# Kernel tuning notes

Measured on AMD Instinct MI355X. Metric: run time of the kernel, lower is better.

The kernel has to match this reference:

```python
import jax, jax.numpy as jnp
import numpy as np

TEMP = 0.5
EPS = 1e-12  # torch F.normalize eps


def setup_inputs() -> dict:
    key = jax.random.key(0)
    k1, k2, k3 = jax.random.split(key, 3)
    B, D = 2048, 128
    z = jax.random.normal(k1, (B, D), dtype=jnp.float32)
    z_aug = jax.random.normal(k2, (B, D), dtype=jnp.float32)
    labels = jax.random.randint(k3, (B,), 0, 2, dtype=jnp.int64)
    return {"z": z, "z_aug": z_aug, "labels": labels}


def _l2_normalize(x):
    n = jnp.linalg.norm(x, axis=1, keepdims=True)
    return x / jnp.maximum(n, EPS)


def _pucon_loss(z, z_aug, labels):
    B = z.shape[0]
    z = _l2_normalize(z)
    z_aug = _l2_normalize(z_aug)

    s00 = (z @ z.T) / TEMP          # [B, B]
    s01 = (z @ z_aug.T) / TEMP
    s10 = (z_aug @ z.T) / TEMP
    s11 = (z_aug @ z_aug.T) / TEMP

    eye = jnp.eye(B, dtype=bool)

    # ---- SelfSupConLoss (reduction='none'): CE over rows with own-diagonal
    # removed from the 00/11 blocks; removal == masking with -inf for CE.
    neg_inf = jnp.array(-jnp.inf, dtype=s00.dtype)
    logits = jnp.concatenate([
        jnp.concatenate([s01, jnp.where(eye, neg_inf, s00)], axis=1),
        jnp.concatenate([s10, jnp.where(eye, neg_inf, s11)], axis=1),
    ], axis=0)                       # [2B, 2B]
    pos = jnp.concatenate([jnp.diagonal(s01), jnp.diagonal(s10)])  # [2B]
    lse = jax.scipy.special.logsumexp(logits, axis=1)
    unsup = lse - pos                # [2B] per-sample NT-Xent loss

    # ---- SupConLoss (reduction='none')
    M = jnp.concatenate([
        jnp.concatenate([s00, s01], axis=1),
        jnp.concatenate([s10, s11], axis=1),
    ], axis=0)                       # [2B, 2B]
    mx = jax.lax.stop_gradient(jnp.max(M, axis=1, keepdims=True))
    Ms = M - mx
    mask = ~jnp.eye(2 * B, dtype=bool)
    e = jnp.where(mask, jnp.exp(Ms), 0.0)
    denom = jnp.sum(e, axis=1, keepdims=True)
    # -log(exp(Ms)/denom) on off-diagonal entries, 0 on diagonal
    nll = jnp.where(mask, jnp.log(denom) - Ms, 0.0)
    eq = labels[:, None] == labels[None, :]
    eq2 = jnp.tile(eq, (2, 2))       # [2B, 2B] bool
    sup = jnp.sum(nll * eq2, axis=1) / (jnp.sum(eq2, axis=1) - 1)  # [2B]

    # ---- PU combination: positives use sup loss, unlabeled use unsup loss
    lab2 = jnp.tile(labels, 2)       # [2B]
    pos_m = (lab2 == 1)
    neg_m = (lab2 == 0)
    n_p = jnp.sum(pos_m)
    n_u = jnp.sum(neg_m)
    total = jnp.maximum(n_p + n_u, 1)
    loss = (jnp.sum(jnp.where(pos_m, sup, 0.0)) +
            jnp.sum(jnp.where(neg_m, unsup, 0.0))) / total
    return jnp.where(n_p == 0, jnp.mean(unsup), loss)


def reference(z, z_aug, labels):
    return _pucon_loss(z, z_aug, labels)
```

## Files before the change

### kernel.cpp

```cpp
#include <hip/hip_runtime.h>
#include <hip/hip_bf16.h>

#define Bsz 2048
#define Dim 128
#define Nrows 4096

typedef float f32x4 __attribute__((ext_vector_type(4)));
typedef __bf16 bf16x8 __attribute__((ext_vector_type(8)));


__global__ __launch_bounds__(256) void k_norm(const float* __restrict__ z,
                                              const float* __restrict__ za,
                                              const long long* __restrict__ labels,
                                              __bf16* __restrict__ U,
                                              float* __restrict__ w1p,
                                              float* __restrict__ wallp,
                                              int* __restrict__ c1out) {
    const int wid = threadIdx.x >> 6, lane = threadIdx.x & 63;
    __shared__ float s1[4][128];
    __shared__ float s0[4][128];
    float a1x = 0.f, a1y = 0.f, a0x = 0.f, a0y = 0.f;
    #pragma unroll
    for (int pass = 0; pass < 4; pass++) {
        const int r = blockIdx.x * 16 + pass * 4 + wid;
        const float* src = (r < Bsz) ? (z + (size_t)r * Dim) : (za + (size_t)(r - Bsz) * Dim);
        float2 x = reinterpret_cast<const float2*>(src)[lane];
        float ss = x.x * x.x + x.y * x.y;
        #pragma unroll
        for (int m = 1; m < 64; m <<= 1) ss += __shfl_xor(ss, m);
        const float sc = 1.0f / fmaxf(sqrtf(ss), 1e-12f);
        const float u0 = x.x * sc, u1 = x.y * sc;
        __bf16* dst = U + (size_t)r * Dim + 2 * lane;
        dst[0] = (__bf16)u0;
        dst[1] = (__bf16)u1;
        const float lf = (labels[r & (Bsz - 1)] == 1) ? 1.f : 0.f;
        a0x += u0; a0y += u1;
        a1x = fmaf(lf, u0, a1x); a1y = fmaf(lf, u1, a1y);
    }
    s1[wid][2 * lane] = a1x; s1[wid][2 * lane + 1] = a1y;
    s0[wid][2 * lane] = a0x; s0[wid][2 * lane + 1] = a0y;
    __syncthreads();
    const int t = threadIdx.x;
    if (t < 128) {
        w1p[blockIdx.x * 128 + t]   = s1[0][t] + s1[1][t] + s1[2][t] + s1[3][t];
        wallp[blockIdx.x * 128 + t] = s0[0][t] + s0[1][t] + s0[2][t] + s0[3][t];
    }
    if (blockIdx.x == 0) {
        __shared__ int ci[256];
        int c = 0;
        #pragma unroll
        for (int k = 0; k < 8; k++) c += (int)labels[t * 8 + k];
        ci[t] = c;
        __syncthreads();
        for (int s = 128; s > 0; s >>= 1) {
            if (t < s) ci[t] += ci[t + s];
            __syncthreads();
        }
        if (t == 0) c1out[0] = ci[0];
    }
}

__global__ __launch_bounds__(512, 2) void k_gram(const __bf16* __restrict__ U,
                                                 const float* __restrict__ w1p,
                                                 const float* __restrict__ wallp,
                                                 float* __restrict__ part,
                                                 float* __restrict__ w1,
                                                 float* __restrict__ wall) {
    if (blockIdx.x == 0) {
        const int t = threadIdx.x;
        if (t < 256) {
            const int d = t & 127;
            const float* src = (t < 128) ? w1p : wallp;
            float acc = 0.f;
            #pragma unroll 8
            for (int k = 0; k < 256; k++) acc += src[k * 128 + d];
            if (t < 128) w1[d] = acc; else wall[d] = acc;
        }
        return;
    }

    __shared__ __bf16 Ai[256 * 128];
    __shared__ __bf16 Aj[256 * 128];

    const int ibk = (blockIdx.x - 1) >> 4, jbk = (blockIdx.x - 1) & 15;
    const bool diag = (ibk == jbk);
    const int ibase = ibk * 256, jbase = jbk * 256;
    const int w = threadIdx.x >> 6, lane = threadIdx.x & 63;
    const int wiq = w & 3, wjh = w >> 2;
    const int l15 = lane & 15, l4 = lane >> 4;

    {
        const int p = lane & 15, rsub = lane >> 4;
        bf16x8 sti[8], stj[8];
        #pragma unroll
        for (int it = 0; it < 8; it++) {
            const int rl = w * 32 + it * 4 + rsub;
            sti[it] = *reinterpret_cast<const bf16x8*>(U + (size_t)(ibase + rl) * Dim + p * 8);
        }
        if (!diag) {
            #pragma unroll
            for (int it = 0; it < 8; it++) {
                const int rl = w * 32 + it * 4 + rsub;
                stj[it] = *reinterpret_cast<const bf16x8*>(U + (size_t)(jbase + rl) * Dim + p * 8);
            }
        }
        #pragma unroll
        for (int it = 0; it < 8; it++) {
            const int rl = w * 32 + it * 4 + rsub;
            *reinterpret_cast<bf16x8*>(Ai + (rl * 16 + (p ^ (rl & 7))) * 8) = sti[it];
        }
        if (!diag) {
            #pragma unroll
            for (int it = 0; it < 8; it++) {
                const int rl = w * 32 + it * 4 + rsub;
                *reinterpret_cast<bf16x8*>(Aj + (rl * 16 + (p ^ (rl & 7))) * 8) = stj[it];
            }
        }
    }
    __syncthreads();
    const __bf16* AjP = diag ? Ai : Aj;

    bf16x8 b[4][4];
    #pragma unroll
    for (int bt = 0; bt < 4; bt++)
        #pragma unroll
        for (int ks = 0; ks < 4; ks++) {
            const int row = wiq * 64 + bt * 16 + l15;
            b[bt][ks] = *reinterpret_cast<const bf16x8*>(
                Ai + (row * 16 + ((ks * 4 + l4) ^ (row & 7))) * 8);
        }

    float dsum[4] = {0.f, 0.f, 0.f, 0.f};
    const float KE1 = 2.8853900817779268f;
    const float KE0 = -2.8853900817779268f;

    #pragma unroll
    for (int at = 0; at < 8; at++) {
        const int arow = wjh * 128 + at * 16 + l15;
        bf16x8 a[4];
        #pragma unroll
        for (int ks = 0; ks < 4; ks++)
            a[ks] = *reinterpret_cast<const bf16x8*>(
                AjP + (arow * 16 + ((ks * 4 + l4) ^ (arow & 7))) * 8);
        const int jt = jbase + wjh * 128 + at * 16;

        #pragma unroll
        for (int bt = 0; bt < 4; bt++) {
            f32x4 acc = {0.f, 0.f, 0.f, 0.f};
            #pragma unroll
            for (int ks = 0; ks < 4; ks++)
                acc = __builtin_amdgcn_mfma_f32_16x16x32_bf16(a[ks], b[bt][ks], acc, 0, 0, 0);
            const bool dg = (jt == ibase + wiq * 64 + bt * 16);
            #pragma unroll
            for (int q = 0; q < 4; q++) {
                float e = exp2f(fmaf(acc[q], KE1, KE0));
                if (dg && (l15 == l4 * 4 + q)) e = 0.f;
                dsum[bt] += e;
            }
        }
    }

    const int strip = jbk * 2 + wjh;
    #pragma unroll
    for (int bt = 0; bt < 4; bt++) {
        float v0 = dsum[bt];
        v0 += __shfl_xor(v0, 16);
        v0 += __shfl_xor(v0, 32);
        if (l4 == 0)
            part[(ibase + wiq * 64 + bt * 16 + l15) * 32 + strip] = v0;
    }
}

__global__ __launch_bounds__(256) void k_row(const __bf16* __restrict__ U,
                                             const long long* __restrict__ labels,
                                             const int* __restrict__ c1p,
                                             const float* __restrict__ part,
                                             const float* __restrict__ w1,
                                             const float* __restrict__ wall,
                                             float* __restrict__ rowC,
                                             float* __restrict__ rowU) {
    const int wid = threadIdx.x >> 6, lane = threadIdx.x & 63;
    const int ls = lane & 31;
    const int c1 = *c1p;
    const float w1a = w1[2 * lane], w1b = w1[2 * lane + 1];
    const float wa  = wall[2 * lane], wb = wall[2 * lane + 1];
    float cs = 0.f, us = 0.f;
    #pragma unroll
    for (int rr = 0; rr < 4; rr++) {
        const int i = blockIdx.x * 16 + wid * 4 + rr;
        const int partner = (i < Bsz) ? i + Bsz : i - Bsz;
        float dn = part[i * 32 + ls];
        const float u0 = (float)U[(size_t)i * Dim + 2 * lane];
        const float u1 = (float)U[(size_t)i * Dim + 2 * lane + 1];
        const float p0 = (float)U[(size_t)partner * Dim + 2 * lane];
        const float p1 = (float)U[(size_t)partner * Dim + 2 * lane + 1];
        float d1 = u0 * w1a + u1 * w1b;
        float da = u0 * wa + u1 * wb;
        float ds = u0 * u0 + u1 * u1;
        float dp = u0 * p0 + u1 * p1;
        #pragma unroll
        for (int m = 1; m < 64; m <<= 1) {
            dn += __shfl_xor(dn, m);
            d1 += __shfl_xor(d1, m);
            da += __shfl_xor(da, m);
            ds += __shfl_xor(ds, m);
            dp += __shfl_xor(dp, m);
        }
        if (lane == 0) {
            const long long lb = labels[i & (Bsz - 1)];
            const float lnD = logf(dn) + 1.30685282f;
            const float uns = lnD - 2.0f * dp;
            const float cnt = 2.f * (float)((lb == 1) ? c1 : (Bsz - c1));
            const float sii = 2.f * ds;
            const float sumeq = ((lb == 1) ? 2.f * d1 : 2.f * (da - d1)) - sii;
            const float sup = lnD - sumeq / (cnt - 1.f);
            cs += (lb == 1) ? sup : uns;
            us += uns;
        }
    }
    __shared__ float wcs[4], wus[4];
    if (lane == 0) { wcs[wid] = cs; wus[wid] = us; }
    __syncthreads();
    if (threadIdx.x == 0) {
        rowC[blockIdx.x] = wcs[0] + wcs[1] + wcs[2] + wcs[3];
        rowU[blockIdx.x] = wus[0] + wus[1] + wus[2] + wus[3];
    }
}

__global__ __launch_bounds__(256) void k_comb(const float* __restrict__ rowC,
                                              const float* __restrict__ rowU,
                                              const int* __restrict__ c1p,
                                              float* __restrict__ out) {
    __shared__ float sc[256], su[256];
    const int t = threadIdx.x;
    sc[t] = rowC[t];
    su[t] = rowU[t];
    __syncthreads();
    for (int s = 128; s > 0; s >>= 1) {
        if (t < s) { sc[t] += sc[t + s]; su[t] += su[t + s]; }
        __syncthreads();
    }
    if (t == 0) out[0] = ((*c1p > 0) ? sc[0] : su[0]) / (float)Nrows;
}

extern "C" void kernel_launch(void* const* d_in, const int* in_sizes, int n_in,
                              void* d_out, int out_size, void* d_ws, size_t ws_size,
                              hipStream_t stream) {
    const float* z  = (const float*)d_in[0];
    const float* za = (const float*)d_in[1];
    const long long* labels = (const long long*)d_in[2];

    char* ws = (char*)d_ws;
    __bf16* U     = (__bf16*)(ws);
    float*  part  = (float*)(ws + (1u << 20));
    float*  w1p   = (float*)(ws + (2u << 20));
    float*  wallp = (float*)(ws + (2u << 20) + (128u << 10));
    float*  w1    = (float*)(ws + (2u << 20) + (256u << 10));
    float*  wall  = (float*)(ws + (2u << 20) + (256u << 10) + 512);
    int*    c1    = (int*)  (ws + (2u << 20) + (256u << 10) + 1024);
    float*  rowC  = (float*)(ws + (2u << 20) + (257u << 10));
    float*  rowU  = (float*)(ws + (2u << 20) + (258u << 10));
    float*  out   = (float*)d_out;

    hipLaunchKernelGGL(k_norm, dim3(256), dim3(256), 0, stream, z, za, labels, U, w1p, wallp, c1);
    hipLaunchKernelGGL(k_gram, dim3(257), dim3(512), 0, stream, U, w1p, wallp, part, w1, wall);
    hipLaunchKernelGGL(k_row,  dim3(256), dim3(256), 0, stream, U, labels, c1, part, w1, wall, rowC, rowU);
    hipLaunchKernelGGL(k_comb, dim3(1),   dim3(256), 0, stream, rowC, rowU, c1, out);
}
```

Before: 32.33 us.

## Fuse L2 normalization into gram kernel and drop separate norm launch

Removes the standalone normalization kernel. Each gram block now reads fp32 z/z_aug directly, normalizes rows on the fly, converts them to bf16 and writes them into shared memory. Diagonal blocks also produce the per-column label-weighted sums. The row kernel recomputes normalized rows and partner rows from fp32 inputs, and the label count moves into the row and combine kernels. This saves one launch and the bf16 intermediate round trip, at the cost of redundant normalization work: each row is normalized by 16 to 32 blocks.

```diff
diff --git a/kernel.cpp b/kernel.cpp
--- a/kernel.cpp
+++ b/kernel.cpp
@@ -7,117 +7,81 @@
 
 typedef float f32x4 __attribute__((ext_vector_type(4)));
 typedef __bf16 bf16x8 __attribute__((ext_vector_type(8)));
-
-
-__global__ __launch_bounds__(256) void k_norm(const float* __restrict__ z,
-                                              const float* __restrict__ za,
-                                              const long long* __restrict__ labels,
-                                              __bf16* __restrict__ U,
-                                              float* __restrict__ w1p,
-                                              float* __restrict__ wallp,
-                                              int* __restrict__ c1out) {
-    const int wid = threadIdx.x >> 6, lane = threadIdx.x & 63;
-    __shared__ float s1[4][128];
-    __shared__ float s0[4][128];
-    float a1x = 0.f, a1y = 0.f, a0x = 0.f, a0y = 0.f;
-    #pragma unroll
-    for (int pass = 0; pass < 4; pass++) {
-        const int r = blockIdx.x * 16 + pass * 4 + wid;
-        const float* src = (r < Bsz) ? (z + (size_t)r * Dim) : (za + (size_t)(r - Bsz) * Dim);
-        float2 x = reinterpret_cast<const float2*>(src)[lane];
-        float ss = x.x * x.x + x.y * x.y;
-        #pragma unroll
-        for (int m = 1; m < 64; m <<= 1) ss += __shfl_xor(ss, m);
-        const float sc = 1.0f / fmaxf(sqrtf(ss), 1e-12f);
-        const float u0 = x.x * sc, u1 = x.y * sc;
-        __bf16* dst = U + (size_t)r * Dim + 2 * lane;
-        dst[0] = (__bf16)u0;
-        dst[1] = (__bf16)u1;
-        const float lf = (labels[r & (Bsz - 1)] == 1) ? 1.f : 0.f;
-        a0x += u0; a0y += u1;
-        a1x = fmaf(lf, u0, a1x); a1y = fmaf(lf, u1, a1y);
-    }
-    s1[wid][2 * lane] = a1x; s1[wid][2 * lane + 1] = a1y;
-    s0[wid][2 * lane] = a0x; s0[wid][2 * lane + 1] = a0y;
-    __syncthreads();
-    const int t = threadIdx.x;
-    if (t < 128) {
-        w1p[blockIdx.x * 128 + t]   = s1[0][t] + s1[1][t] + s1[2][t] + s1[3][t];
-        wallp[blockIdx.x * 128 + t] = s0[0][t] + s0[1][t] + s0[2][t] + s0[3][t];
-    }
-    if (blockIdx.x == 0) {
-        __shared__ int ci[256];
-        int c = 0;
-        #pragma unroll
-        for (int k = 0; k < 8; k++) c += (int)labels[t * 8 + k];
-        ci[t] = c;
-        __syncthreads();
-        for (int s = 128; s > 0; s >>= 1) {
-            if (t < s) ci[t] += ci[t + s];
-            __syncthreads();
-        }
-        if (t == 0) c1out[0] = ci[0];
-    }
-}
-
-__global__ __launch_bounds__(512, 2) void k_gram(const __bf16* __restrict__ U,
-                                                 const float* __restrict__ w1p,
-                                                 const float* __restrict__ wallp,
+typedef __bf16 bf16x4 __attribute__((ext_vector_type(4)));
+
+
+__global__ __launch_bounds__(512, 2) void k_gram(const float* __restrict__ z,
+                                                 const float* __restrict__ za,
+                                                 const long long* __restrict__ labels,
                                                  float* __restrict__ part,
-                                                 float* __restrict__ w1,
-                                                 float* __restrict__ wall) {
-    if (blockIdx.x == 0) {
-        const int t = threadIdx.x;
-        if (t < 256) {
-            const int d = t & 127;
-            const float* src = (t < 128) ? w1p : wallp;
-            float acc = 0.f;
-            #pragma unroll 8
-            for (int k = 0; k < 256; k++) acc += src[k * 128 + d];
-            if (t < 128) w1[d] = acc; else wall[d] = acc;
-        }
-        return;
-    }
-
+                                                 float* __restrict__ w1p,
+                                                 float* __restrict__ wallp) {
     __shared__ __bf16 Ai[256 * 128];
     __shared__ __bf16 Aj[256 * 128];
 
-    const int ibk = (blockIdx.x - 1) >> 4, jbk = (blockIdx.x - 1) & 15;
+    const int ibk = blockIdx.x >> 4, jbk = blockIdx.x & 15;
     const bool diag = (ibk == jbk);
     const int ibase = ibk * 256, jbase = jbk * 256;
     const int w = threadIdx.x >> 6, lane = threadIdx.x & 63;
     const int wiq = w & 3, wjh = w >> 2;
     const int l15 = lane & 15, l4 = lane >> 4;
-
-    {
-        const int p = lane & 15, rsub = lane >> 4;
-        bf16x8 sti[8], stj[8];
-        #pragma unroll
-        for (int it = 0; it < 8; it++) {
-            const int rl = w * 32 + it * 4 + rsub;
-            sti[it] = *reinterpret_cast<const bf16x8*>(U + (size_t)(ibase + rl) * Dim + p * 8);
+    const int half = lane >> 5, l32 = lane & 31;
+    const int g = w * 2 + half;
+    float* scr = reinterpret_cast<float*>(Aj);
+
+    float a1[4] = {0.f, 0.f, 0.f, 0.f}, a0[4] = {0.f, 0.f, 0.f, 0.f};
+    const int p = l32 >> 1;
+    #pragma unroll
+    for (int it = 0; it < 16; it++) {
+        const int rl = it * 16 + g;
+        {
+            const int r = ibase + rl;
+            const float* src = (r < Bsz) ? (z + (size_t)r * Dim) : (za + (size_t)(r - Bsz) * Dim);
+            f32x4 x = *reinterpret_cast<const f32x4*>(src + l32 * 4);
+            float ss = x[0]*x[0] + x[1]*x[1] + x[2]*x[2] + x[3]*x[3];
+            ss += __shfl_xor(ss, 1); ss += __shfl_xor(ss, 2); ss += __shfl_xor(ss, 4);
+            ss += __shfl_xor(ss, 8); ss += __shfl_xor(ss, 16);
+            const float sc = 1.0f / fmaxf(sqrtf(ss), 1e-12f);
+            const float u0 = x[0]*sc, u1 = x[1]*sc, u2 = x[2]*sc, u3 = x[3]*sc;
+            bf16x4 b4 = {(__bf16)u0, (__bf16)u1, (__bf16)u2, (__bf16)u3};
+            *reinterpret_cast<bf16x4*>(Ai + (rl * 16 + (p ^ (rl & 7))) * 8 + (l32 & 1) * 4) = b4;
+            if (diag) {
+                const float lf = (labels[r & (Bsz - 1)] == 1) ? 1.f : 0.f;
+                a0[0] += u0; a0[1] += u1; a0[2] += u2; a0[3] += u3;
+                a1[0] = fmaf(lf, u0, a1[0]); a1[1] = fmaf(lf, u1, a1[1]);
+                a1[2] = fmaf(lf, u2, a1[2]); a1[3] = fmaf(lf, u3, a1[3]);
+            }
         }
         if (!diag) {
-            #pragma unroll
-            for (int it = 0; it < 8; it++) {
-                const int rl = w * 32 + it * 4 + rsub;
-                stj[it] = *reinterpret_cast<const bf16x8*>(U + (size_t)(jbase + rl) * Dim + p * 8);
-            }
-        }
-        #pragma unroll
-        for (int it = 0; it < 8; it++) {
-            const int rl = w * 32 + it * 4 + rsub;
-            *reinterpret_cast<bf16x8*>(Ai + (rl * 16 + (p ^ (rl & 7))) * 8) = sti[it];
-        }
-        if (!diag) {
-            #pragma unroll
-            for (int it = 0; it < 8; it++) {
-                const int rl = w * 32 + it * 4 + rsub;
-                *reinterpret_cast<bf16x8*>(Aj + (rl * 16 + (p ^ (rl & 7))) * 8) = stj[it];
-            }
-        }
-    }
-    __syncthreads();
+            const int r = jbase + rl;
+            const float* src = (r < Bsz) ? (z + (size_t)r * Dim) : (za + (size_t)(r - Bsz) * Dim);
+            f32x4 x = *reinterpret_cast<const f32x4*>(src + l32 * 4);
+            float ss = x[0]*x[0] + x[1]*x[1] + x[2]*x[2] + x[3]*x[3];
+            ss += __shfl_xor(ss, 1); ss += __shfl_xor(ss, 2); ss += __shfl_xor(ss, 4);
+            ss += __shfl_xor(ss, 8); ss += __shfl_xor(ss, 16);
+            const float sc = 1.0f / fmaxf(sqrtf(ss), 1e-12f);
+            bf16x4 b4 = {(__bf16)(x[0]*sc), (__bf16)(x[1]*sc), (__bf16)(x[2]*sc), (__bf16)(x[3]*sc)};
+            *reinterpret_cast<bf16x4*>(Aj + (rl * 16 + (p ^ (rl & 7))) * 8 + (l32 & 1) * 4) = b4;
+        }
+    }
+    if (diag) {
+        #pragma unroll
+        for (int k2 = 0; k2 < 4; k2++) {
+            scr[g * 128 + l32 * 4 + k2]        = a1[k2];
+            scr[2048 + g * 128 + l32 * 4 + k2] = a0[k2];
+        }
+    }
+    __syncthreads();
+
+    if (diag && threadIdx.x < 256) {
+        const int d = threadIdx.x & 127;
+        const int which = threadIdx.x >> 7;
+        float acc = 0.f;
+        #pragma unroll
+        for (int gg = 0; gg < 16; gg++) acc += scr[which * 2048 + gg * 128 + d];
+        (which ? wallp : w1p)[ibk * 128 + d] = acc;
+    }
+
     const __bf16* AjP = diag ? Ai : Aj;
 
     bf16x8 b[4][4];
@@ -171,29 +135,72 @@
     }
 }
 
-__global__ __launch_bounds__(256) void k_row(const __bf16* __restrict__ U,
+__global__ __launch_bounds__(256) void k_row(const float* __restrict__ z,
+                                             const float* __restrict__ za,
                                              const long long* __restrict__ labels,
-                                             const int* __restrict__ c1p,
                                              const float* __restrict__ part,
-                                             const float* __restrict__ w1,
-                                             const float* __restrict__ wall,
+                                             const float* __restrict__ w1p,
+                                             const float* __restrict__ wallp,
                                              float* __restrict__ rowC,
                                              float* __restrict__ rowU) {
-    const int wid = threadIdx.x >> 6, lane = threadIdx.x & 63;
+    __shared__ float sw1[128], sw0[128];
+    __shared__ int ci[256];
+    __shared__ int sc1v;
+    const int t = threadIdx.x;
+    if (t < 128) {
+        float a = 0.f;
+        #pragma unroll
+        for (int gg = 0; gg < 16; gg++) a += w1p[gg * 128 + t];
+        sw1[t] = a;
+    } else {
+        const int d = t - 128;
+        float a = 0.f;
+        #pragma unroll
+        for (int gg = 0; gg < 16; gg++) a += wallp[gg * 128 + d];
+        sw0[d] = a;
+    }
+    {
+        int c = 0;
+        #pragma unroll
+        for (int k = 0; k < 8; k++) c += (int)labels[t * 8 + k];
+        ci[t] = c;
+    }
+    __syncthreads();
+    for (int s = 128; s > 0; s >>= 1) {
+        if (t < s) ci[t] += ci[t + s];
+        __syncthreads();
+    }
+    if (t == 0) sc1v = ci[0];
+    __syncthreads();
+
+    const int wid = t >> 6, lane = t & 63;
     const int ls = lane & 31;
-    const int c1 = *c1p;
-    const float w1a = w1[2 * lane], w1b = w1[2 * lane + 1];
-    const float wa  = wall[2 * lane], wb = wall[2 * lane + 1];
+    const int c1 = sc1v;
+    const float w1a = sw1[2 * lane], w1b = sw1[2 * lane + 1];
+    const float wa  = sw0[2 * lane], wb = sw0[2 * lane + 1];
     float cs = 0.f, us = 0.f;
     #pragma unroll
     for (int rr = 0; rr < 4; rr++) {
         const int i = blockIdx.x * 16 + wid * 4 + rr;
         const int partner = (i < Bsz) ? i + Bsz : i - Bsz;
+        const float* si = (i < Bsz) ? (z + (size_t)i * Dim) : (za + (size_t)(i - Bsz) * Dim);
+        const float* sp = (partner < Bsz) ? (z + (size_t)partner * Dim)
+                                          : (za + (size_t)(partner - Bsz) * Dim);
+        const float2 xi = reinterpret_cast<const float2*>(si)[lane];
+        const float2 xp = reinterpret_cast<const float2*>(sp)[lane];
+        float ssi = xi.x * xi.x + xi.y * xi.y;
+        float ssp = xp.x * xp.x + xp.y * xp.y;
+        #pragma unroll
+        for (int m = 1; m < 64; m <<= 1) {
+            ssi += __shfl_xor(ssi, m);
+            ssp += __shfl_xor(ssp, m);
+        }
+        const float sci = 1.0f / fmaxf(sqrtf(ssi), 1e-12f);
+        const float scp = 1.0f / fmaxf(sqrtf(ssp), 1e-12f);
+        const float u0 = (float)(__bf16)(xi.x * sci), u1 = (float)(__bf16)(xi.y * sci);
+        const float p0 = (float)(__bf16)(xp.x * scp), p1 = (float)(__bf16)(xp.y * scp);
+
         float dn = part[i * 32 + ls];
-        const float u0 = (float)U[(size_t)i * Dim + 2 * lane];
-        const float u1 = (float)U[(size_t)i * Dim + 2 * lane + 1];
-        const float p0 = (float)U[(size_t)partner * Dim + 2 * lane];
-        const float p1 = (float)U[(size_t)partner * Dim + 2 * lane + 1];
         float d1 = u0 * w1a + u1 * w1b;
         float da = u0 * wa + u1 * wb;
         float ds = u0 * u0 + u1 * u1;
@@ -221,7 +228,7 @@
     __shared__ float wcs[4], wus[4];
     if (lane == 0) { wcs[wid] = cs; wus[wid] = us; }
     __syncthreads();
-    if (threadIdx.x == 0) {
+    if (t == 0) {
         rowC[blockIdx.x] = wcs[0] + wcs[1] + wcs[2] + wcs[3];
         rowU[blockIdx.x] = wus[0] + wus[1] + wus[2] + wus[3];
     }
@@ -229,18 +236,25 @@
 
 __global__ __launch_bounds__(256) void k_comb(const float* __restrict__ rowC,
                                               const float* __restrict__ rowU,
-                                              const int* __restrict__ c1p,
+                                              const long long* __restrict__ labels,
                                               float* __restrict__ out) {
     __shared__ float sc[256], su[256];
+    __shared__ int ci[256];
     const int t = threadIdx.x;
     sc[t] = rowC[t];
     su[t] = rowU[t];
+    {
+        int c = 0;
+        #pragma unroll
+        for (int k = 0; k < 8; k++) c += (int)labels[t * 8 + k];
+        ci[t] = c;
+    }
     __syncthreads();
     for (int s = 128; s > 0; s >>= 1) {
-        if (t < s) { sc[t] += sc[t + s]; su[t] += su[t + s]; }
+        if (t < s) { sc[t] += sc[t + s]; su[t] += su[t + s]; ci[t] += ci[t + s]; }
         __syncthreads();
     }
-    if (t == 0) out[0] = ((*c1p > 0) ? sc[0] : su[0]) / (float)Nrows;
+    if (t == 0) out[0] = ((ci[0] > 0) ? sc[0] : su[0]) / (float)Nrows;
 }
 
 extern "C" void kernel_launch(void* const* d_in, const int* in_sizes, int n_in,
@@ -251,19 +265,14 @@
     const long long* labels = (const long long*)d_in[2];
 
     char* ws = (char*)d_ws;
-    __bf16* U     = (__bf16*)(ws);
-    float*  part  = (float*)(ws + (1u << 20));
-    float*  w1p   = (float*)(ws + (2u << 20));
-    float*  wallp = (float*)(ws + (2u << 20) + (128u << 10));
-    float*  w1    = (float*)(ws + (2u << 20) + (256u << 10));
-    float*  wall  = (float*)(ws + (2u << 20) + (256u << 10) + 512);
-    int*    c1    = (int*)  (ws + (2u << 20) + (256u << 10) + 1024);
-    float*  rowC  = (float*)(ws + (2u << 20) + (257u << 10));
-    float*  rowU  = (float*)(ws + (2u << 20) + (258u << 10));
-    float*  out   = (float*)d_out;
-
-    hipLaunchKernelGGL(k_norm, dim3(256), dim3(256), 0, stream, z, za, labels, U, w1p, wallp, c1);
-    hipLaunchKernelGGL(k_gram, dim3(257), dim3(512), 0, stream, U, w1p, wallp, part, w1, wall);
-    hipLaunchKernelGGL(k_row,  dim3(256), dim3(256), 0, stream, U, labels, c1, part, w1, wall, rowC, rowU);
-    hipLaunchKernelGGL(k_comb, dim3(1),   dim3(256), 0, stream, rowC, rowU, c1, out);
-}
+    float* part  = (float*)(ws);
+    float* w1p   = (float*)(ws + (512u << 10));
+    float* wallp = (float*)(ws + (512u << 10) + (8u << 10));
+    float* rowC  = (float*)(ws + (512u << 10) + (16u << 10));
+    float* rowU  = (float*)(ws + (512u << 10) + (17u << 10));
+    float* out   = (float*)d_out;
+
+    hipLaunchKernelGGL(k_gram, dim3(256), dim3(512), 0, stream, z, za, labels, part, w1p, wallp);
+    hipLaunchKernelGGL(k_row,  dim3(256), dim3(256), 0, stream, z, za, labels, part, w1p, wallp, rowC, rowU);
+    hipLaunchKernelGGL(k_comb, dim3(1),   dim3(256), 0, stream, rowC, rowU, labels, out);
+}
```

Result: slower. 34.69 us (+7.3%).
